# Kernel optimization log

Hardware: AMD Instinct MI355X
Metric: run time of the kernel (lower is better)

## Reference

```python
import jax, jax.numpy as jnp
import numpy as np

DIM = 768
HEADS = 16
HEAD_DIM = DIM // HEADS  # 48


def setup_inputs() -> dict:
    key = jax.random.key(0)
    ks = jax.random.split(key, 9)
    s = 1.0 / np.sqrt(DIM)
    inp = {
        "x": jax.random.normal(ks[0], (4, 2048, DIM), dtype=jnp.float32),
        "Wq": jax.random.uniform(ks[1], (DIM, DIM), jnp.float32, -s, s),
        "bq": jax.random.uniform(ks[2], (DIM,), jnp.float32, -s, s),
        "Wk": jax.random.uniform(ks[3], (DIM, DIM), jnp.float32, -s, s),
        "bk": jax.random.uniform(ks[4], (DIM,), jnp.float32, -s, s),
        "Wv": jax.random.uniform(ks[5], (DIM, DIM), jnp.float32, -s, s),
        "bv": jax.random.uniform(ks[6], (DIM,), jnp.float32, -s, s),
        "Wo": jax.random.uniform(ks[7], (DIM, DIM), jnp.float32, -s, s),
        "bo": jax.random.uniform(ks[8], (DIM,), jnp.float32, -s, s),
    }
    return inp


def reference(x, Wq, bq, Wk, bk, Wv, bv, Wo, bo):
    B, S, _ = x.shape
    # torch nn.Linear: y = x @ W.T + b
    q = x @ Wq.T + bq
    k = x @ Wk.T + bk
    v = x @ Wv.T + bv
    # split heads: (B, H, S, Dh)
    q = q.reshape(B, S, HEADS, HEAD_DIM).transpose(0, 2, 1, 3)
    k = k.reshape(B, S, HEADS, HEAD_DIM).transpose(0, 2, 1, 3)
    v = v.reshape(B, S, HEADS, HEAD_DIM).transpose(0, 2, 1, 3)
    score = jnp.einsum("bhqd,bhkd->bhqk", q, k) / jnp.sqrt(jnp.float32(HEAD_DIM))
    attn = jax.nn.softmax(score, axis=-1)
    out = jnp.einsum("bhqk,bhkd->bhqd", attn, v)
    out = out.transpose(0, 2, 1, 3).reshape(B, S, DIM)
    return out @ Wo.T + bo
```

## Files before the change

kernel.cpp:

```cpp
#include <hip/hip_runtime.h>

#define DIM 768
#define SEQ 2048
#define NB 4
#define NH 16
#define DH 48
#define DP 64
#define BHN (NB*NH)
#define MTOK (NB*SEQ)

typedef __attribute__((ext_vector_type(8))) short bf16x8;
typedef __attribute__((ext_vector_type(4))) float f32x4;
typedef __attribute__((ext_vector_type(4))) unsigned int u32x4;

__device__ __forceinline__ unsigned short f32_to_bf16(float f) {
    union { float f; unsigned int u; } v; v.f = f;
    unsigned int r = v.u + 0x7fff + ((v.u >> 16) & 1);
    return (unsigned short)(r >> 16);
}

#if __has_builtin(__builtin_amdgcn_exp2f)
#define EXP2F(x) __builtin_amdgcn_exp2f(x)
#else
#define EXP2F(x) exp2f(x)
#endif

#define GL_LDS16(g, l) __builtin_amdgcn_global_load_lds( \
    (const __attribute__((address_space(1))) void*)(g),  \
    (__attribute__((address_space(3))) void*)(l), 16, 0, 0)

__global__ void cvt_f32_bf16(const float* __restrict__ src, unsigned short* __restrict__ dst, int n) {
    int i = (blockIdx.x * blockDim.x + threadIdx.x) * 4;
    if (i + 3 < n) {
        const float4 v = *(const float4*)(src + i);
        ushort4 o;
        o.x = f32_to_bf16(v.x); o.y = f32_to_bf16(v.y);
        o.z = f32_to_bf16(v.z); o.w = f32_to_bf16(v.w);
        *(ushort4*)(dst + i) = o;
    }
}

__global__ void cvt4_f32_bf16(const float* __restrict__ a, const float* __restrict__ b,
                              const float* __restrict__ c, const float* __restrict__ d,
                              unsigned short* __restrict__ dst, int n_each) {
    const float* srcs[4] = {a, b, c, d};
    const float* src = srcs[blockIdx.y];
    unsigned short* out = dst + blockIdx.y * n_each;
    int i = (blockIdx.x * blockDim.x + threadIdx.x) * 4;
    if (i + 3 < n_each) {
        const float4 v = *(const float4*)(src + i);
        ushort4 o;
        o.x = f32_to_bf16(v.x); o.y = f32_to_bf16(v.y);
        o.z = f32_to_bf16(v.z); o.w = f32_to_bf16(v.w);
        *(ushort4*)(out + i) = o;
    }
}

#define BK 32

__global__ __launch_bounds__(256) void qkv_gemm(
    const unsigned short* __restrict__ xb,
    const unsigned short* __restrict__ wb,
    const float* __restrict__ bq, const float* __restrict__ bk, const float* __restrict__ bv,
    unsigned short* __restrict__ Qb, unsigned short* __restrict__ Kb, unsigned short* __restrict__ Vt)
{
    const int z = blockIdx.z;
    const unsigned short* W = wb + z * (DIM * DIM);
    const float* bias = (z == 0) ? bq : (z == 1) ? bk : bv;
    const int row0 = blockIdx.x * 128;
    const int col0 = blockIdx.y * 128;

    __shared__ __align__(16) short As[128 * BK];
    __shared__ __align__(16) short Bs[128 * BK];

    const int tid = threadIdx.x;
    const int lane = tid & 63;
    const int w = tid >> 6;
    const int wy = w >> 1, wx = w & 1;
    const int l15 = lane & 15, quad = lane >> 4;
    const int lr = lane >> 2;
    const int lco = (lane & 3) * 8;

    f32x4 acc[4][4];
    for (int mi = 0; mi < 4; ++mi) for (int ni = 0; ni < 4; ++ni)
        for (int r = 0; r < 4; ++r) acc[mi][ni][r] = 0.f;

    for (int kt = 0; kt < DIM / BK; ++kt) {
        #pragma unroll
        for (int j = 0; j < 2; ++j) {
            const int c = w * 2 + j;
            GL_LDS16(&xb[(row0 + c * 16 + lr) * DIM + kt * BK + lco], &As[c * 512]);
            GL_LDS16(&W [(col0 + c * 16 + lr) * DIM + kt * BK + lco], &Bs[c * 512]);
        }
        __syncthreads();
        bf16x8 af[4], bfr[4];
        #pragma unroll
        for (int mi = 0; mi < 4; ++mi)
            af[mi] = *(const bf16x8*)&As[(wy * 64 + mi * 16 + l15) * BK + quad * 8];
        #pragma unroll
        for (int ni = 0; ni < 4; ++ni)
            bfr[ni] = *(const bf16x8*)&Bs[(wx * 64 + ni * 16 + l15) * BK + quad * 8];
        #pragma unroll
        for (int mi = 0; mi < 4; ++mi)
            #pragma unroll
            for (int ni = 0; ni < 4; ++ni)
                acc[mi][ni] = __builtin_amdgcn_mfma_f32_16x16x32_bf16(af[mi], bfr[ni], acc[mi][ni], 0, 0, 0);
        __syncthreads();
    }

    const float qscale = 0.14433756729740643f * 1.4426950408889634f;

    if (z == 2) {
        #pragma unroll
        for (int mi = 0; mi < 4; ++mi) {
            #pragma unroll
            for (int ni = 0; ni < 4; ++ni) {
                int col = col0 + wx * 64 + ni * 16 + l15;
                int h = col / DH, d = col - h * DH;
                int row = row0 + wy * 64 + mi * 16 + quad * 4;
                int b = row >> 11, s = row & 2047;
                float bi = bias[col];
                union { ushort4 v; unsigned short e[4]; } pk;
                #pragma unroll
                for (int r = 0; r < 4; ++r)
                    pk.e[r] = f32_to_bf16(acc[mi][ni][r] + bi);
                *(ushort4*)&Vt[((b * NH + h) * DP + d) * SEQ + s] = pk.v;
            }
        }
    } else {
        #pragma unroll
        for (int mi = 0; mi < 4; ++mi) {
            #pragma unroll
            for (int ni = 0; ni < 4; ++ni) {
                #pragma unroll
                for (int r = 0; r < 4; ++r) {
                    int row = row0 + wy * 64 + mi * 16 + quad * 4 + r;
                    int col = col0 + wx * 64 + ni * 16 + l15;
                    float v = acc[mi][ni][r] + bias[col];
                    int b = row >> 11, s = row & 2047;
                    int h = col / DH, d = col - h * DH;
                    int bh = b * NH + h;
                    if (z == 0) Qb[(bh * SEQ + s) * DP + d] = f32_to_bf16(v * qscale);
                    else        Kb[(bh * SEQ + s) * DP + d] = f32_to_bf16(v);
                }
            }
        }
    }
}

__global__ __launch_bounds__(256) void out_gemm(
    const unsigned short* __restrict__ ab,
    const unsigned short* __restrict__ Wo,
    const float* __restrict__ bo,
    float* __restrict__ out)
{
    const int row0 = blockIdx.x * 128;
    const int col0 = blockIdx.y * 128;

    __shared__ __align__(16) short As[128 * BK];
    __shared__ __align__(16) short Bs[128 * BK];

    const int tid = threadIdx.x;
    const int lane = tid & 63;
    const int w = tid >> 6;
    const int wy = w >> 1, wx = w & 1;
    const int l15 = lane & 15, quad = lane >> 4;
    const int lr = lane >> 2;
    const int lco = (lane & 3) * 8;

    f32x4 acc[4][4];
    for (int mi = 0; mi < 4; ++mi) for (int ni = 0; ni < 4; ++ni)
        for (int r = 0; r < 4; ++r) acc[mi][ni][r] = 0.f;

    for (int kt = 0; kt < DIM / BK; ++kt) {
        #pragma unroll
        for (int j = 0; j < 2; ++j) {
            const int c = w * 2 + j;
            GL_LDS16(&ab[(row0 + c * 16 + lr) * DIM + kt * BK + lco], &As[c * 512]);
            GL_LDS16(&Wo[(col0 + c * 16 + lr) * DIM + kt * BK + lco], &Bs[c * 512]);
        }
        __syncthreads();
        bf16x8 af[4], bfr[4];
        #pragma unroll
        for (int mi = 0; mi < 4; ++mi)
            af[mi] = *(const bf16x8*)&As[(wy * 64 + mi * 16 + l15) * BK + quad * 8];
        #pragma unroll
        for (int ni = 0; ni < 4; ++ni)
            bfr[ni] = *(const bf16x8*)&Bs[(wx * 64 + ni * 16 + l15) * BK + quad * 8];
        #pragma unroll
        for (int mi = 0; mi < 4; ++mi)
            #pragma unroll
            for (int ni = 0; ni < 4; ++ni)
                acc[mi][ni] = __builtin_amdgcn_mfma_f32_16x16x32_bf16(af[mi], bfr[ni], acc[mi][ni], 0, 0, 0);
        __syncthreads();
    }

    #pragma unroll
    for (int mi = 0; mi < 4; ++mi)
        #pragma unroll
        for (int ni = 0; ni < 4; ++ni)
            #pragma unroll
            for (int r = 0; r < 4; ++r) {
                int row = row0 + wy * 64 + mi * 16 + quad * 4 + r;
                int col = col0 + wx * 64 + ni * 16 + l15;
                out[row * DIM + col] = acc[mi][ni][r] + bo[col];
            }
}

__device__ __forceinline__ int keyperm(int a) {
    return (a & 32) + ((a & 12) << 1) + ((a & 16) >> 2) + (a & 3);
}

__global__ __launch_bounds__(256, 2) void attn_kernel(
    const unsigned short* __restrict__ Qb,
    const unsigned short* __restrict__ Kb,
    const unsigned short* __restrict__ Vt,
    unsigned short* __restrict__ Ob)
{
    const int bh = blockIdx.x;
    const int tile = blockIdx.y;
    const int tid = threadIdx.x;
    const int w = tid >> 6;
    const int lane = tid & 63;
    const int l15 = lane & 15, quad = lane >> 4;

    const unsigned short* Qh = Qb + bh * SEQ * DP;
    const unsigned short* Kh = Kb + bh * SEQ * DP;
    const unsigned short* Vh = Vt + bh * DP * SEQ;
    const int q0 = tile * 256 + w * 64;

    __shared__ __align__(16) short Ks[64 * 64];
    __shared__ __align__(16) short Vs[48 * 64];

    bf16x8 aq[4][2];
    #pragma unroll
    for (int m = 0; m < 4; ++m)
        #pragma unroll
        for (int ks = 0; ks < 2; ++ks)
            aq[m][ks] = *(const bf16x8*)&Qh[(q0 + m * 16 + l15) * DP + ks * 32 + quad * 8];
    if (quad >= 2) {
        const bf16x8 z8 = {0, 0, 0, 0, 0, 0, 0, 0};
        #pragma unroll
        for (int m = 0; m < 4; ++m) aq[m][1] = z8;
    }

    f32x4 o[4][3];
    #pragma unroll
    for (int m = 0; m < 4; ++m) for (int ni = 0; ni < 3; ++ni)
        for (int r = 0; r < 4; ++r) o[m][ni][r] = 0.f;
    float ls[4][2];
    #pragma unroll
    for (int m = 0; m < 4; ++m) { ls[m][0] = 0.f; ls[m][1] = 0.f; }

    const f32x4 FZ = {0.f, 0.f, 0.f, 0.f};

    const int ra = tid >> 2;
    const int pc = tid & 3;
    const int lcA = ((pc ^ (ra & 7)) * 8);
    const int lcB = (((pc + 4) ^ (ra & 7)) * 8);
    const int kaR = keyperm(ra);
    const int ldsA = ra * 64 + pc * 8;
    const int ldsB = ra * 64 + (pc + 4) * 8;
    const bool vld = (tid < 192);

    bf16x8 kr0, kr1, vr0, vr1;
    kr0 = *(const bf16x8*)&Kh[kaR * DP + lcA];
    kr1 = *(const bf16x8*)&Kh[kaR * DP + lcB];
    if (vld) {
        vr0 = *(const bf16x8*)&Vh[ra * SEQ + lcA];
        vr1 = *(const bf16x8*)&Vh[ra * SEQ + lcB];
    }

    for (int kt = 0; kt < SEQ / 64; ++kt) {
        __syncthreads();
        *(bf16x8*)&Ks[ldsA] = kr0;
        *(bf16x8*)&Ks[ldsB] = kr1;
        if (vld) {
            *(bf16x8*)&Vs[ldsA] = vr0;
            *(bf16x8*)&Vs[ldsB] = vr1;
        }
        if (kt + 1 < SEQ / 64) {
            const int k0n = (kt + 1) * 64;
            kr0 = *(const bf16x8*)&Kh[(k0n + kaR) * DP + lcA];
            kr1 = *(const bf16x8*)&Kh[(k0n + kaR) * DP + lcB];
            if (vld) {
                vr0 = *(const bf16x8*)&Vh[ra * SEQ + k0n + lcA];
                vr1 = *(const bf16x8*)&Vh[ra * SEQ + k0n + lcB];
            }
        }
        __syncthreads();

        bf16x8 ak0[4], ak1[4];
        #pragma unroll
        for (int n = 0; n < 4; ++n) {
            ak0[n] = *(const bf16x8*)&Ks[(n * 16 + l15) * 64 + ((quad ^ (l15 & 7)) * 8)];
            ak1[n] = *(const bf16x8*)&Ks[(n * 16 + l15) * 64 + (((4 + quad) ^ (l15 & 7)) * 8)];
        }
        bf16x8 av[2][3];
        #pragma unroll
        for (int ks = 0; ks < 2; ++ks)
            #pragma unroll
            for (int mt = 0; mt < 3; ++mt)
                av[ks][mt] = *(const bf16x8*)&Vs[(mt * 16 + l15) * 64 + (((ks * 4 + quad) ^ (l15 & 7)) * 8)];

        #pragma unroll
        for (int mp = 0; mp < 2; ++mp) {
            const int m0 = 2 * mp, m1 = 2 * mp + 1;
            f32x4 sc[2][4];
            #pragma unroll
            for (int n = 0; n < 4; ++n) {
                sc[0][n] = __builtin_amdgcn_mfma_f32_16x16x32_bf16(ak0[n], aq[m0][0], FZ, 0, 0, 0);
                sc[1][n] = __builtin_amdgcn_mfma_f32_16x16x32_bf16(ak0[n], aq[m1][0], FZ, 0, 0, 0);
            }
            #pragma unroll
            for (int n = 0; n < 4; ++n) {
                sc[0][n] = __builtin_amdgcn_mfma_f32_16x16x32_bf16(ak1[n], aq[m0][1], sc[0][n], 0, 0, 0);
                sc[1][n] = __builtin_amdgcn_mfma_f32_16x16x32_bf16(ak1[n], aq[m1][1], sc[1][n], 0, 0, 0);
            }
            union { u32x4 u; bf16x8 h; } bp[2][2];
            #pragma unroll
            for (int mi = 0; mi < 2; ++mi) {
                #pragma unroll
                for (int ks = 0; ks < 2; ++ks) {
                    #pragma unroll
                    for (int w2 = 0; w2 < 4; ++w2) {
                        const int j0 = 2 * w2, j1 = 2 * w2 + 1;
                        float p0 = EXP2F(sc[mi][2 * ks + (j0 >> 2)][j0 & 3]);
                        float p1 = EXP2F(sc[mi][2 * ks + (j1 >> 2)][j1 & 3]);
                        ls[2 * mp + mi][w2 & 1] += (p0 + p1);
                        bp[mi][ks].u[w2] = __builtin_amdgcn_perm(__float_as_uint(p1), __float_as_uint(p0), 0x07060302u);
                    }
                }
            }
            #pragma unroll
            for (int ks = 0; ks < 2; ++ks)
                #pragma unroll
                for (int mt = 0; mt < 3; ++mt) {
                    o[m0][mt] = __builtin_amdgcn_mfma_f32_16x16x32_bf16(av[ks][mt], bp[0][ks].h, o[m0][mt], 0, 0, 0);
                    o[m1][mt] = __builtin_amdgcn_mfma_f32_16x16x32_bf16(av[ks][mt], bp[1][ks].h, o[m1][mt], 0, 0, 0);
                }
        }
    }

    const int b = bh >> 4, h = bh & 15;
    #pragma unroll
    for (int m = 0; m < 4; ++m) {
        float lsum = ls[m][0] + ls[m][1];
        lsum += __shfl_xor(lsum, 16);
        lsum += __shfl_xor(lsum, 32);
        float inv = 1.f / lsum;
        #pragma unroll
        for (int mt = 0; mt < 3; ++mt)
            #pragma unroll
            for (int r = 0; r < 4; ++r) {
                int token = b * SEQ + q0 + m * 16 + l15;
                int d = mt * 16 + quad * 4 + r;
                Ob[token * DIM + h * DH + d] = f32_to_bf16(o[m][mt][r] * inv);
            }
    }
}

extern "C" void kernel_launch(void* const* d_in, const int* in_sizes, int n_in,
                              void* d_out, int out_size, void* d_ws, size_t ws_size,
                              hipStream_t stream) {
    const float* x  = (const float*)d_in[0];
    const float* Wq = (const float*)d_in[1]; const float* bq = (const float*)d_in[2];
    const float* Wk = (const float*)d_in[3]; const float* bk = (const float*)d_in[4];
    const float* Wv = (const float*)d_in[5]; const float* bv = (const float*)d_in[6];
    const float* Wo = (const float*)d_in[7]; const float* bo = (const float*)d_in[8];

    unsigned char* ws = (unsigned char*)d_ws;
    unsigned short* xb = (unsigned short*)(ws);
    unsigned short* wb = (unsigned short*)(ws + 12582912);
    unsigned short* Qb = (unsigned short*)(ws + 17301504);
    unsigned short* Kb = (unsigned short*)(ws + 34078720);
    unsigned short* Vt = (unsigned short*)(ws + 50855936);
    unsigned short* Ob = (unsigned short*)(ws + 67633152);

    cvt_f32_bf16<<<6144, 256, 0, stream>>>(x, xb, MTOK * DIM);
    cvt4_f32_bf16<<<dim3(576, 4), 256, 0, stream>>>(Wq, Wk, Wv, Wo, wb, DIM * DIM);

    qkv_gemm<<<dim3(MTOK / 128, DIM / 128, 3), 256, 0, stream>>>(xb, wb, bq, bk, bv, Qb, Kb, Vt);
    attn_kernel<<<dim3(BHN, SEQ / 256), 256, 0, stream>>>(Qb, Kb, Vt, Ob);
    out_gemm<<<dim3(MTOK / 128, DIM / 128), 256, 0, stream>>>(Ob, wb + 3 * DIM * DIM, bo, (float*)d_out);
}
```

Measured before the change: 218.9 us.

## Double-buffer GEMM tiles, fold softmax row-sum into PV MFMA via ones column

Both projection GEMMs now double-buffer their LDS tiles, so the global-to-LDS load of the next K-slice overlaps the MFMAs on the current one. The attention kernel pads V to 64 rows and sets row 48 to ones in a new init kernel, so the PV MFMA produces the softmax denominator and the per-element row-sum adds and shuffles go away. It also adds s_setprio around the MFMA blocks, drops the occupancy hint from launch bounds, and vectorises the output stores. The cost is a third more PV MFMA work, an extra launch, and a larger LDS footprint.

```diff
diff --git a/kernel.cpp b/kernel.cpp
--- a/kernel.cpp
+++ b/kernel.cpp
@@ -56,6 +56,15 @@
     }
 }
 
+__global__ void vt_pad_init(unsigned short* __restrict__ Vt) {
+    const int bhd = blockIdx.x;
+    const int d = 48 + blockIdx.y;
+    const unsigned short val = (blockIdx.y == 0) ? (unsigned short)0x3F80 : (unsigned short)0;
+    ushort4 v4 = {val, val, val, val};
+    ushort4* dst = (ushort4*)&Vt[(bhd * DP + d) * SEQ];
+    for (int i = threadIdx.x; i < SEQ / 4; i += 256) dst[i] = v4;
+}
+
 #define BK 32
 
 __global__ __launch_bounds__(256) void qkv_gemm(
@@ -70,8 +79,8 @@
     const int row0 = blockIdx.x * 128;
     const int col0 = blockIdx.y * 128;
 
-    __shared__ __align__(16) short As[128 * BK];
-    __shared__ __align__(16) short Bs[128 * BK];
+    __shared__ __align__(16) short As[2][128 * BK];
+    __shared__ __align__(16) short Bs[2][128 * BK];
 
     const int tid = threadIdx.x;
     const int lane = tid & 63;
@@ -85,26 +94,37 @@
     for (int mi = 0; mi < 4; ++mi) for (int ni = 0; ni < 4; ++ni)
         for (int r = 0; r < 4; ++r) acc[mi][ni][r] = 0.f;
 
-    for (int kt = 0; kt < DIM / BK; ++kt) {
-        #pragma unroll
-        for (int j = 0; j < 2; ++j) {
-            const int c = w * 2 + j;
-            GL_LDS16(&xb[(row0 + c * 16 + lr) * DIM + kt * BK + lco], &As[c * 512]);
-            GL_LDS16(&W [(col0 + c * 16 + lr) * DIM + kt * BK + lco], &Bs[c * 512]);
-        }
-        __syncthreads();
-        bf16x8 af[4], bfr[4];
-        #pragma unroll
-        for (int mi = 0; mi < 4; ++mi)
-            af[mi] = *(const bf16x8*)&As[(wy * 64 + mi * 16 + l15) * BK + quad * 8];
-        #pragma unroll
-        for (int ni = 0; ni < 4; ++ni)
-            bfr[ni] = *(const bf16x8*)&Bs[(wx * 64 + ni * 16 + l15) * BK + quad * 8];
-        #pragma unroll
-        for (int mi = 0; mi < 4; ++mi)
-            #pragma unroll
-            for (int ni = 0; ni < 4; ++ni)
-                acc[mi][ni] = __builtin_amdgcn_mfma_f32_16x16x32_bf16(af[mi], bfr[ni], acc[mi][ni], 0, 0, 0);
+#define QKV_STAGE(B, KT) do { \
+    _Pragma("unroll") \
+    for (int j = 0; j < 2; ++j) { \
+        const int c = w * 2 + j; \
+        GL_LDS16(&xb[(row0 + c * 16 + lr) * DIM + (KT) * BK + lco], &As[B][c * 512]); \
+        GL_LDS16(&W [(col0 + c * 16 + lr) * DIM + (KT) * BK + lco], &Bs[B][c * 512]); \
+    } } while (0)
+
+#define QKV_COMPUTE(B) do { \
+    bf16x8 af[4], bfr[4]; \
+    _Pragma("unroll") \
+    for (int mi = 0; mi < 4; ++mi) \
+        af[mi] = *(const bf16x8*)&As[B][(wy * 64 + mi * 16 + l15) * BK + quad * 8]; \
+    _Pragma("unroll") \
+    for (int ni = 0; ni < 4; ++ni) \
+        bfr[ni] = *(const bf16x8*)&Bs[B][(wx * 64 + ni * 16 + l15) * BK + quad * 8]; \
+    _Pragma("unroll") \
+    for (int mi = 0; mi < 4; ++mi) \
+        _Pragma("unroll") \
+        for (int ni = 0; ni < 4; ++ni) \
+            acc[mi][ni] = __builtin_amdgcn_mfma_f32_16x16x32_bf16(af[mi], bfr[ni], acc[mi][ni], 0, 0, 0); \
+    } while (0)
+
+    QKV_STAGE(0, 0);
+    __syncthreads();
+    for (int kt = 0; kt < DIM / BK; kt += 2) {
+        QKV_STAGE(1, kt + 1);
+        QKV_COMPUTE(0);
+        __syncthreads();
+        if (kt + 2 < DIM / BK) QKV_STAGE(0, kt + 2);
+        QKV_COMPUTE(1);
         __syncthreads();
     }
 
@@ -157,8 +177,8 @@
     const int row0 = blockIdx.x * 128;
     const int col0 = blockIdx.y * 128;
 
-    __shared__ __align__(16) short As[128 * BK];
-    __shared__ __align__(16) short Bs[128 * BK];
+    __shared__ __align__(16) short As[2][128 * BK];
+    __shared__ __align__(16) short Bs[2][128 * BK];
 
     const int tid = threadIdx.x;
     const int lane = tid & 63;
@@ -172,26 +192,22 @@
     for (int mi = 0; mi < 4; ++mi) for (int ni = 0; ni < 4; ++ni)
         for (int r = 0; r < 4; ++r) acc[mi][ni][r] = 0.f;
 
-    for (int kt = 0; kt < DIM / BK; ++kt) {
-        #pragma unroll
-        for (int j = 0; j < 2; ++j) {
-            const int c = w * 2 + j;
-            GL_LDS16(&ab[(row0 + c * 16 + lr) * DIM + kt * BK + lco], &As[c * 512]);
-            GL_LDS16(&Wo[(col0 + c * 16 + lr) * DIM + kt * BK + lco], &Bs[c * 512]);
-        }
-        __syncthreads();
-        bf16x8 af[4], bfr[4];
-        #pragma unroll
-        for (int mi = 0; mi < 4; ++mi)
-            af[mi] = *(const bf16x8*)&As[(wy * 64 + mi * 16 + l15) * BK + quad * 8];
-        #pragma unroll
-        for (int ni = 0; ni < 4; ++ni)
-            bfr[ni] = *(const bf16x8*)&Bs[(wx * 64 + ni * 16 + l15) * BK + quad * 8];
-        #pragma unroll
-        for (int mi = 0; mi < 4; ++mi)
-            #pragma unroll
-            for (int ni = 0; ni < 4; ++ni)
-                acc[mi][ni] = __builtin_amdgcn_mfma_f32_16x16x32_bf16(af[mi], bfr[ni], acc[mi][ni], 0, 0, 0);
+#define OUT_STAGE(B, KT) do { \
+    _Pragma("unroll") \
+    for (int j = 0; j < 2; ++j) { \
+        const int c = w * 2 + j; \
+        GL_LDS16(&ab[(row0 + c * 16 + lr) * DIM + (KT) * BK + lco], &As[B][c * 512]); \
+        GL_LDS16(&Wo[(col0 + c * 16 + lr) * DIM + (KT) * BK + lco], &Bs[B][c * 512]); \
+    } } while (0)
+
+    OUT_STAGE(0, 0);
+    __syncthreads();
+    for (int kt = 0; kt < DIM / BK; kt += 2) {
+        OUT_STAGE(1, kt + 1);
+        QKV_COMPUTE(0);
+        __syncthreads();
+        if (kt + 2 < DIM / BK) OUT_STAGE(0, kt + 2);
+        QKV_COMPUTE(1);
         __syncthreads();
     }
 
@@ -211,7 +227,7 @@
     return (a & 32) + ((a & 12) << 1) + ((a & 16) >> 2) + (a & 3);
 }
 
-__global__ __launch_bounds__(256, 2) void attn_kernel(
+__global__ __launch_bounds__(256) void attn_kernel(
     const unsigned short* __restrict__ Qb,
     const unsigned short* __restrict__ Kb,
     const unsigned short* __restrict__ Vt,
@@ -230,7 +246,7 @@
     const int q0 = tile * 256 + w * 64;
 
     __shared__ __align__(16) short Ks[64 * 64];
-    __shared__ __align__(16) short Vs[48 * 64];
+    __shared__ __align__(16) short Vs[64 * 64];
 
     bf16x8 aq[4][2];
     #pragma unroll
@@ -244,49 +260,38 @@
         for (int m = 0; m < 4; ++m) aq[m][1] = z8;
     }
 
-    f32x4 o[4][3];
+    f32x4 o[4][4];
     #pragma unroll
-    for (int m = 0; m < 4; ++m) for (int ni = 0; ni < 3; ++ni)
+    for (int m = 0; m < 4; ++m) for (int ni = 0; ni < 4; ++ni)
         for (int r = 0; r < 4; ++r) o[m][ni][r] = 0.f;
-    float ls[4][2];
-    #pragma unroll
-    for (int m = 0; m < 4; ++m) { ls[m][0] = 0.f; ls[m][1] = 0.f; }
 
     const f32x4 FZ = {0.f, 0.f, 0.f, 0.f};
 
-    const int ra = tid >> 2;
-    const int pc = tid & 3;
-    const int lcA = ((pc ^ (ra & 7)) * 8);
-    const int lcB = (((pc + 4) ^ (ra & 7)) * 8);
+    const int ra = tid >> 3;
+    const int pc = tid & 7;
+    const int lc = (pc ^ (ra & 7)) * 8;
     const int kaR = keyperm(ra);
     const int ldsA = ra * 64 + pc * 8;
-    const int ldsB = ra * 64 + (pc + 4) * 8;
-    const bool vld = (tid < 192);
+    const int ldsB = ldsA + 32 * 64;
 
     bf16x8 kr0, kr1, vr0, vr1;
-    kr0 = *(const bf16x8*)&Kh[kaR * DP + lcA];
-    kr1 = *(const bf16x8*)&Kh[kaR * DP + lcB];
-    if (vld) {
-        vr0 = *(const bf16x8*)&Vh[ra * SEQ + lcA];
-        vr1 = *(const bf16x8*)&Vh[ra * SEQ + lcB];
-    }
+    kr0 = *(const bf16x8*)&Kh[kaR * DP + lc];
+    kr1 = *(const bf16x8*)&Kh[(kaR + 32) * DP + lc];
+    vr0 = *(const bf16x8*)&Vh[ra * SEQ + lc];
+    vr1 = *(const bf16x8*)&Vh[(ra + 32) * SEQ + lc];
 
     for (int kt = 0; kt < SEQ / 64; ++kt) {
         __syncthreads();
         *(bf16x8*)&Ks[ldsA] = kr0;
         *(bf16x8*)&Ks[ldsB] = kr1;
-        if (vld) {
-            *(bf16x8*)&Vs[ldsA] = vr0;
-            *(bf16x8*)&Vs[ldsB] = vr1;
-        }
+        *(bf16x8*)&Vs[ldsA] = vr0;
+        *(bf16x8*)&Vs[ldsB] = vr1;
         if (kt + 1 < SEQ / 64) {
             const int k0n = (kt + 1) * 64;
-            kr0 = *(const bf16x8*)&Kh[(k0n + kaR) * DP + lcA];
-            kr1 = *(const bf16x8*)&Kh[(k0n + kaR) * DP + lcB];
-            if (vld) {
-                vr0 = *(const bf16x8*)&Vh[ra * SEQ + k0n + lcA];
-                vr1 = *(const bf16x8*)&Vh[ra * SEQ + k0n + lcB];
-            }
+            kr0 = *(const bf16x8*)&Kh[(k0n + kaR) * DP + lc];
+            kr1 = *(const bf16x8*)&Kh[(k0n + kaR + 32) * DP + lc];
+            vr0 = *(const bf16x8*)&Vh[ra * SEQ + k0n + lc];
+            vr1 = *(const bf16x8*)&Vh[(ra + 32) * SEQ + k0n + lc];
         }
         __syncthreads();
 
@@ -296,17 +301,18 @@
             ak0[n] = *(const bf16x8*)&Ks[(n * 16 + l15) * 64 + ((quad ^ (l15 & 7)) * 8)];
             ak1[n] = *(const bf16x8*)&Ks[(n * 16 + l15) * 64 + (((4 + quad) ^ (l15 & 7)) * 8)];
         }
-        bf16x8 av[2][3];
+        bf16x8 av[2][4];
         #pragma unroll
         for (int ks = 0; ks < 2; ++ks)
             #pragma unroll
-            for (int mt = 0; mt < 3; ++mt)
+            for (int mt = 0; mt < 4; ++mt)
                 av[ks][mt] = *(const bf16x8*)&Vs[(mt * 16 + l15) * 64 + (((ks * 4 + quad) ^ (l15 & 7)) * 8)];
 
         #pragma unroll
         for (int mp = 0; mp < 2; ++mp) {
             const int m0 = 2 * mp, m1 = 2 * mp + 1;
             f32x4 sc[2][4];
+            __builtin_amdgcn_s_setprio(1);
             #pragma unroll
             for (int n = 0; n < 4; ++n) {
                 sc[0][n] = __builtin_amdgcn_mfma_f32_16x16x32_bf16(ak0[n], aq[m0][0], FZ, 0, 0, 0);
@@ -317,6 +323,7 @@
                 sc[0][n] = __builtin_amdgcn_mfma_f32_16x16x32_bf16(ak1[n], aq[m0][1], sc[0][n], 0, 0, 0);
                 sc[1][n] = __builtin_amdgcn_mfma_f32_16x16x32_bf16(ak1[n], aq[m1][1], sc[1][n], 0, 0, 0);
             }
+            __builtin_amdgcn_s_setprio(0);
             union { u32x4 u; bf16x8 h; } bp[2][2];
             #pragma unroll
             for (int mi = 0; mi < 2; ++mi) {
@@ -327,36 +334,36 @@
                         const int j0 = 2 * w2, j1 = 2 * w2 + 1;
                         float p0 = EXP2F(sc[mi][2 * ks + (j0 >> 2)][j0 & 3]);
                         float p1 = EXP2F(sc[mi][2 * ks + (j1 >> 2)][j1 & 3]);
-                        ls[2 * mp + mi][w2 & 1] += (p0 + p1);
                         bp[mi][ks].u[w2] = __builtin_amdgcn_perm(__float_as_uint(p1), __float_as_uint(p0), 0x07060302u);
                     }
                 }
             }
+            __builtin_amdgcn_s_setprio(1);
             #pragma unroll
             for (int ks = 0; ks < 2; ++ks)
                 #pragma unroll
-                for (int mt = 0; mt < 3; ++mt) {
+                for (int mt = 0; mt < 4; ++mt) {
                     o[m0][mt] = __builtin_amdgcn_mfma_f32_16x16x32_bf16(av[ks][mt], bp[0][ks].h, o[m0][mt], 0, 0, 0);
                     o[m1][mt] = __builtin_amdgcn_mfma_f32_16x16x32_bf16(av[ks][mt], bp[1][ks].h, o[m1][mt], 0, 0, 0);
                 }
+            __builtin_amdgcn_s_setprio(0);
         }
     }
 
     const int b = bh >> 4, h = bh & 15;
     #pragma unroll
     for (int m = 0; m < 4; ++m) {
-        float lsum = ls[m][0] + ls[m][1];
-        lsum += __shfl_xor(lsum, 16);
-        lsum += __shfl_xor(lsum, 32);
+        float lsum = __shfl(o[m][3][0], l15);
         float inv = 1.f / lsum;
-        #pragma unroll
-        for (int mt = 0; mt < 3; ++mt)
-            #pragma unroll
-            for (int r = 0; r < 4; ++r) {
-                int token = b * SEQ + q0 + m * 16 + l15;
-                int d = mt * 16 + quad * 4 + r;
-                Ob[token * DIM + h * DH + d] = f32_to_bf16(o[m][mt][r] * inv);
-            }
+        int token = b * SEQ + q0 + m * 16 + l15;
+        #pragma unroll
+        for (int mt = 0; mt < 3; ++mt) {
+            union { ushort4 v; unsigned short e[4]; } pk;
+            #pragma unroll
+            for (int r = 0; r < 4; ++r)
+                pk.e[r] = f32_to_bf16(o[m][mt][r] * inv);
+            *(ushort4*)&Ob[token * DIM + h * DH + mt * 16 + quad * 4] = pk.v;
+        }
     }
 }
 
@@ -379,6 +386,7 @@
 
     cvt_f32_bf16<<<6144, 256, 0, stream>>>(x, xb, MTOK * DIM);
     cvt4_f32_bf16<<<dim3(576, 4), 256, 0, stream>>>(Wq, Wk, Wv, Wo, wb, DIM * DIM);
+    vt_pad_init<<<dim3(BHN, 16), 256, 0, stream>>>(Vt);
 
     qkv_gemm<<<dim3(MTOK / 128, DIM / 128, 3), 256, 0, stream>>>(xb, wb, bq, bk, bv, Qb, Kb, Vt);
     attn_kernel<<<dim3(BHN, SEQ / 256), 256, 0, stream>>>(Qb, Kb, Vt, Ob);
```

New measurement: 271.4 us. 24.0% more time.
